# Kernel optimization log

Hardware: AMD Instinct MI355X
Metric: run time of the kernel (lower is better)

## Reference

```python
import jax, jax.numpy as jnp
import numpy as np
import math

H = 1024      # hidden_size
NH = 32       # nhead
DH = H // NH  # head dim (== NH by construction, required for broadcasting)
SF = 0.2      # scaling_factor
B, S = 1, 48  # batch, seq_len (Sq == Sk required)


def setup_inputs() -> dict:
    key = jax.random.key(0)
    ks = jax.random.split(key, 9)
    sd = 1.0 / math.sqrt(H)
    return {
        "q": jax.random.normal(ks[0], (B, S, H), jnp.float32),
        "k": jax.random.normal(ks[1], (B, S, H), jnp.float32),
        "v": jax.random.normal(ks[2], (B, S, H), jnp.float32),
        "Wq": jax.random.normal(ks[3], (H, H), jnp.float32) * sd,
        "bq": jax.random.normal(ks[4], (H,), jnp.float32) * sd,
        "Wk": jax.random.normal(ks[5], (H, H), jnp.float32) * sd,
        "bk": jax.random.normal(ks[6], (H,), jnp.float32) * sd,
        "Wv": jax.random.normal(ks[7], (H, H), jnp.float32) * sd,
        "bv": jax.random.normal(ks[8], (H,), jnp.float32) * sd,
        "dropout_p": 0,
    }


def reference(q, k, v, Wq, bq, Wk, bk, Wv, bv, dropout_p):
    inv_sqrt_h = 1.0 / math.sqrt(H)
    qp = q @ Wq.T + bq  # [B,S,H]
    kp = k @ Wk.T + bk
    vp = v @ Wv.T + bv

    def heads(x):
        # view(-1, S, NH, DH).transpose(0,1) -> [S, B, NH, DH]
        return jnp.swapaxes(x.reshape(-1, x.shape[1], NH, DH), 0, 1)

    qh = heads(qp) * inv_sqrt_h          # [S,B,NH,DH]
    kh = heads(kp)
    vh = heads(vp)

    _sq = jnp.sum(qh * qh, axis=-1)      # [S,B,NH]
    # k^T @ q over the head axis: [S,B,DH,NH] @ [S,B,NH,DH] -> [S,B,DH,DH]
    _sk = jnp.matmul(jnp.swapaxes(kh, -1, -2), qh) * inv_sqrt_h

    # broadcast: [S,B,NH,1] + [S,B,DH,DH,1] + |[S,B,DH,DH]-[S,B,NH,1]|*SF
    # with B=1, DH==NH -> _s: [S,S,NH,NH,NH]
    _s = (_sq[..., None] + _sk[..., None]
          + jnp.abs(jnp.swapaxes(_sk, -1, -2) - _sq[..., None]) * SF)
    attn = jax.nn.softmax(_s, axis=-1)   # [S,S,NH,NH,NH]
    # dropout_p == 0 -> identity (matches `if dropout_p > 0` in torch source)

    out = jnp.matmul(attn, vh)           # batch-broadcast matmul -> [S,S,NH,NH,NH]
    out = jnp.swapaxes(out, 0, 1)
    return out.reshape(out.shape[1], -1)  # [S, S*NH^3]
```

## Files before the change

kernel.cpp:

```cpp
#include <hip/hip_runtime.h>

constexpr int kH  = 1024;
constexpr int kS  = 48;
constexpr int kNH = 32;
constexpr int kDH = 32;
constexpr float kSF = 0.2f;
constexpr int kRepsPerRow = kS * kNH;
constexpr int kRowF4      = kRepsPerRow * 256;

typedef float f32x4 __attribute__((ext_vector_type(4)));

__device__ __forceinline__ float4 ld4(const float* p) {
    return *reinterpret_cast<const float4*>(p);
}
__device__ __forceinline__ float dot4(float4 a, float4 b) {
    return a.x * b.x + a.y * b.y + a.z * b.z + a.w * b.w;
}

__global__ __launch_bounds__(256) void proj_kernel(
    const float* __restrict__ q, const float* __restrict__ k, const float* __restrict__ v,
    const float* __restrict__ Wq, const float* __restrict__ bq,
    const float* __restrict__ Wk, const float* __restrict__ bk,
    const float* __restrict__ Wv, const float* __restrict__ bv,
    float* __restrict__ ws)
{
    const int wid  = blockIdx.x * 4 + (threadIdx.x >> 6);
    const int lane = threadIdx.x & 63;
    const int g = wid >> 10;
    const int o = wid & 1023;

    const float *X, *W, *Bv;
    if (g == 0)      { X = q; W = Wq; Bv = bq; }
    else if (g == 1) { X = k; W = Wk; Bv = bk; }
    else             { X = v; W = Wv; Bv = bv; }
    float* OUT = ws + g * (kS * kH);

    const float* wr = W + o * kH + lane * 4;
    const float4 w0 = ld4(wr);
    const float4 w1 = ld4(wr + 256);
    const float4 w2 = ld4(wr + 512);
    const float4 w3 = ld4(wr + 768);

    float acc[kS];
#pragma unroll
    for (int s = 0; s < kS; ++s) {
        const float* xr = X + s * kH + lane * 4;
        float4 x0 = ld4(xr);
        float4 x1 = ld4(xr + 256);
        float4 x2 = ld4(xr + 512);
        float4 x3 = ld4(xr + 768);
        acc[s] = dot4(x0, w0) + dot4(x1, w1) + dot4(x2, w2) + dot4(x3, w3);
    }
#pragma unroll
    for (int s = 0; s < kS; ++s) {
        float a = acc[s];
        a += __shfl_xor(a, 1);
        a += __shfl_xor(a, 2);
        a += __shfl_xor(a, 4);
        a += __shfl_xor(a, 8);
        a += __shfl_xor(a, 16);
        a += __shfl_xor(a, 32);
        acc[s] = a;
    }
    if (lane == 0) {
        const float bo = Bv[o];
#pragma unroll
        for (int s = 0; s < kS; ++s) OUT[s * kH + o] = acc[s] + bo;
    }
}

__global__ __launch_bounds__(256) void attn_kernel(
    const float* __restrict__ ws, float* __restrict__ O)
{
    const int s = blockIdx.x;
    const int t = threadIdx.x;

    __shared__ float qrow[kH];
    __shared__ float krow[kH];
    __shared__ float vrow[kH];
    __shared__ float sq[kNH];
    __shared__ float sk[kDH][kDH];
    __shared__ float pT[kNH][kNH];

    const float* qp = ws;
    const float* kp = ws + kS * kH;
    const float* vp = ws + 2 * kS * kH;

    reinterpret_cast<float4*>(qrow)[t] = ld4(qp + s * kH + t * 4);
    reinterpret_cast<float4*>(krow)[t] = ld4(kp + s * kH + t * 4);
    reinterpret_cast<float4*>(vrow)[t] = ld4(vp + s * kH + t * 4);
    __syncthreads();

    if (t < kNH) {
        float a = 0.f;
#pragma unroll
        for (int d = 0; d < kDH; ++d) {
            float x = qrow[t * kDH + d];
            a += x * x;
        }
        sq[t] = a * (1.0f / 1024.0f);
    }
    {
        const int d = t >> 3;
        const int eq = t & 7;
        float4 a = {0.f, 0.f, 0.f, 0.f};
#pragma unroll
        for (int n = 0; n < kNH; ++n) {
            const float kv = krow[n * kDH + d];
            const float4 qv = reinterpret_cast<const float4*>(qrow)[n * 8 + eq];
            a.x += kv * qv.x; a.y += kv * qv.y; a.z += kv * qv.z; a.w += kv * qv.w;
        }
        const float sc = 1.0f / 1024.0f;
        a.x *= sc; a.y *= sc; a.z *= sc; a.w *= sc;
        *reinterpret_cast<float4*>(&sk[d][eq * 4]) = a;
    }
    __syncthreads();

    {
        const int b = t >> 3;
        const int c0 = (t & 7) * 4;
        const float s0 = sq[b];
        float v0 = kSF * fabsf(sk[c0 + 0][b] - s0);
        float v1 = kSF * fabsf(sk[c0 + 1][b] - s0);
        float v2 = kSF * fabsf(sk[c0 + 2][b] - s0);
        float v3 = kSF * fabsf(sk[c0 + 3][b] - s0);
        float m = fmaxf(fmaxf(v0, v1), fmaxf(v2, v3));
        m = fmaxf(m, __shfl_xor(m, 1));
        m = fmaxf(m, __shfl_xor(m, 2));
        m = fmaxf(m, __shfl_xor(m, 4));
        float e0 = __expf(v0 - m);
        float e1 = __expf(v1 - m);
        float e2 = __expf(v2 - m);
        float e3 = __expf(v3 - m);
        float sum = e0 + e1 + e2 + e3;
        sum += __shfl_xor(sum, 1);
        sum += __shfl_xor(sum, 2);
        sum += __shfl_xor(sum, 4);
        const float inv = 1.0f / sum;
        pT[c0 + 0][b] = e0 * inv;
        pT[c0 + 1][b] = e1 * inv;
        pT[c0 + 2][b] = e2 * inv;
        pT[c0 + 3][b] = e3 * inv;
    }
    __syncthreads();

    {
        const int b = t >> 3;
        const int dq = t & 7;
        float4 acc = {0.f, 0.f, 0.f, 0.f};
#pragma unroll
        for (int c = 0; c < kNH; ++c) {
            const float pv = pT[c][b];
            const float4 vv = reinterpret_cast<const float4*>(vrow)[c * 8 + dq];
            acc.x += pv * vv.x; acc.y += pv * vv.y; acc.z += pv * vv.z; acc.w += pv * vv.w;
        }
        reinterpret_cast<float4*>(O + s * kH + b * kDH)[dq] = acc;
    }
}

__global__ __launch_bounds__(256) void bcast_kernel(
    const float* __restrict__ O, float* __restrict__ out)
{
    const int x  = blockIdx.x / 96;
    const int rb = blockIdx.x % 96;
    const int t  = threadIdx.x;

    const f32x4 v = *reinterpret_cast<const f32x4*>(O + x * kH + t * 4);
    f32x4* dst = reinterpret_cast<f32x4*>(out)
               + (size_t)x * kRowF4 + (size_t)rb * (16 * 256) + t;
#pragma unroll
    for (int i = 0; i < 16; ++i) {
        __builtin_nontemporal_store(v, dst + i * 256);
    }
}

extern "C" void kernel_launch(void* const* d_in, const int* in_sizes, int n_in,
                              void* d_out, int out_size, void* d_ws, size_t ws_size,
                              hipStream_t stream)
{
    (void)in_sizes; (void)n_in; (void)out_size; (void)ws_size;
    const float* q  = (const float*)d_in[0];
    const float* k  = (const float*)d_in[1];
    const float* v  = (const float*)d_in[2];
    const float* Wq = (const float*)d_in[3];
    const float* bq = (const float*)d_in[4];
    const float* Wk = (const float*)d_in[5];
    const float* bk = (const float*)d_in[6];
    const float* Wv = (const float*)d_in[7];
    const float* bv = (const float*)d_in[8];

    float* ws  = (float*)d_ws;
    float* O   = ws + 3 * kS * kH;
    float* out = (float*)d_out;

    proj_kernel<<<768, 256, 0, stream>>>(q, k, v, Wq, bq, Wk, bk, Wv, bv, ws);
    attn_kernel<<<kS, 256, 0, stream>>>(ws, O);
    bcast_kernel<<<kS * 96, 256, 0, stream>>>(O, out);
}
```

Baseline: 89.69 us.

## Fuse attention into broadcast kernel and tile projection X through shared memory

The projection kernel now stages 128-column tiles of X in shared memory and assigns 32 lanes per output row, so each block computes 8 outputs while reusing the staged X. The attention kernel is merged with the broadcast writer: each of 48*32 blocks recomputes the per-row attention and then writes 48 replicated rows. This removes one launch and the intermediate O buffer. The cost is recomputing attention 32 times per row, and the output stores become ordinary stores instead of nontemporal ones.

```diff
diff --git a/kernel.cpp b/kernel.cpp
--- a/kernel.cpp
+++ b/kernel.cpp
@@ -8,8 +8,6 @@
 constexpr int kRepsPerRow = kS * kNH;
 constexpr int kRowF4      = kRepsPerRow * 256;
 
-typedef float f32x4 __attribute__((ext_vector_type(4)));
-
 __device__ __forceinline__ float4 ld4(const float* p) {
     return *reinterpret_cast<const float4*>(p);
 }
@@ -24,10 +22,12 @@
     const float* __restrict__ Wv, const float* __restrict__ bv,
     float* __restrict__ ws)
 {
-    const int wid  = blockIdx.x * 4 + (threadIdx.x >> 6);
-    const int lane = threadIdx.x & 63;
-    const int g = wid >> 10;
-    const int o = wid & 1023;
+    const int bid = blockIdx.x;
+    const int t = threadIdx.x;
+    const int g = bid >> 7;
+    const int otile = bid & 127;
+    const int o = otile * 8 + (t >> 5);
+    const int kg = t & 31;
 
     const float *X, *W, *Bv;
     if (g == 0)      { X = q; W = Wq; Bv = bq; }
@@ -35,22 +35,31 @@
     else             { X = v; W = Wv; Bv = bv; }
     float* OUT = ws + g * (kS * kH);
 
-    const float* wr = W + o * kH + lane * 4;
-    const float4 w0 = ld4(wr);
-    const float4 w1 = ld4(wr + 256);
-    const float4 w2 = ld4(wr + 512);
-    const float4 w3 = ld4(wr + 768);
+    __shared__ float Xs[kS][128];
 
     float acc[kS];
 #pragma unroll
-    for (int s = 0; s < kS; ++s) {
-        const float* xr = X + s * kH + lane * 4;
-        float4 x0 = ld4(xr);
-        float4 x1 = ld4(xr + 256);
-        float4 x2 = ld4(xr + 512);
-        float4 x3 = ld4(xr + 768);
-        acc[s] = dot4(x0, w0) + dot4(x1, w1) + dot4(x2, w2) + dot4(x3, w3);
-    }
+    for (int s = 0; s < kS; ++s) acc[s] = 0.f;
+
+    for (int kt = 0; kt < 8; ++kt) {
+#pragma unroll
+        for (int r = 0; r < 6; ++r) {
+            const int fi = r * 256 + t;
+            const int s  = fi >> 5;
+            const int c  = fi & 31;
+            reinterpret_cast<float4*>(&Xs[s][0])[c] = ld4(X + s * kH + kt * 128 + c * 4);
+        }
+        __syncthreads();
+
+        const float4 wv = ld4(W + o * kH + kt * 128 + kg * 4);
+#pragma unroll
+        for (int s = 0; s < kS; ++s) {
+            const float4 xv = reinterpret_cast<const float4*>(&Xs[s][0])[kg];
+            acc[s] += dot4(xv, wv);
+        }
+        __syncthreads();
+    }
+
 #pragma unroll
     for (int s = 0; s < kS; ++s) {
         float a = acc[s];
@@ -59,21 +68,21 @@
         a += __shfl_xor(a, 4);
         a += __shfl_xor(a, 8);
         a += __shfl_xor(a, 16);
-        a += __shfl_xor(a, 32);
         acc[s] = a;
     }
-    if (lane == 0) {
+    if (kg == 0) {
         const float bo = Bv[o];
 #pragma unroll
         for (int s = 0; s < kS; ++s) OUT[s * kH + o] = acc[s] + bo;
     }
 }
 
-__global__ __launch_bounds__(256) void attn_kernel(
-    const float* __restrict__ ws, float* __restrict__ O)
+__global__ __launch_bounds__(256) void fused_kernel(
+    const float* __restrict__ ws, float* __restrict__ out)
 {
-    const int s = blockIdx.x;
-    const int t = threadIdx.x;
+    const int x  = blockIdx.x >> 5;
+    const int rb = blockIdx.x & 31;
+    const int t  = threadIdx.x;
 
     __shared__ float qrow[kH];
     __shared__ float krow[kH];
@@ -81,22 +90,23 @@
     __shared__ float sq[kNH];
     __shared__ float sk[kDH][kDH];
     __shared__ float pT[kNH][kNH];
+    __shared__ float Osh[kH];
 
     const float* qp = ws;
     const float* kp = ws + kS * kH;
     const float* vp = ws + 2 * kS * kH;
 
-    reinterpret_cast<float4*>(qrow)[t] = ld4(qp + s * kH + t * 4);
-    reinterpret_cast<float4*>(krow)[t] = ld4(kp + s * kH + t * 4);
-    reinterpret_cast<float4*>(vrow)[t] = ld4(vp + s * kH + t * 4);
+    reinterpret_cast<float4*>(qrow)[t] = ld4(qp + x * kH + t * 4);
+    reinterpret_cast<float4*>(krow)[t] = ld4(kp + x * kH + t * 4);
+    reinterpret_cast<float4*>(vrow)[t] = ld4(vp + x * kH + t * 4);
     __syncthreads();
 
     if (t < kNH) {
         float a = 0.f;
 #pragma unroll
         for (int d = 0; d < kDH; ++d) {
-            float x = qrow[t * kDH + d];
-            a += x * x;
+            float xq = qrow[t * kDH + d];
+            a += xq * xq;
         }
         sq[t] = a * (1.0f / 1024.0f);
     }
@@ -154,23 +164,18 @@
             const float4 vv = reinterpret_cast<const float4*>(vrow)[c * 8 + dq];
             acc.x += pv * vv.x; acc.y += pv * vv.y; acc.z += pv * vv.z; acc.w += pv * vv.w;
         }
-        reinterpret_cast<float4*>(O + s * kH + b * kDH)[dq] = acc;
-    }
-}
-
-__global__ __launch_bounds__(256) void bcast_kernel(
-    const float* __restrict__ O, float* __restrict__ out)
-{
-    const int x  = blockIdx.x / 96;
-    const int rb = blockIdx.x % 96;
-    const int t  = threadIdx.x;
-
-    const f32x4 v = *reinterpret_cast<const f32x4*>(O + x * kH + t * 4);
-    f32x4* dst = reinterpret_cast<f32x4*>(out)
-               + (size_t)x * kRowF4 + (size_t)rb * (16 * 256) + t;
-#pragma unroll
-    for (int i = 0; i < 16; ++i) {
-        __builtin_nontemporal_store(v, dst + i * 256);
+        reinterpret_cast<float4*>(Osh + b * kDH)[dq] = acc;
+    }
+    __syncthreads();
+
+    {
+        const float4 v = reinterpret_cast<const float4*>(Osh)[t];
+        float4* dst = reinterpret_cast<float4*>(out)
+                    + (size_t)x * kRowF4 + (size_t)rb * (48 * 256) + t;
+#pragma unroll
+        for (int i = 0; i < 48; ++i) {
+            dst[i * 256] = v;
+        }
     }
 }
 
@@ -190,10 +195,8 @@
     const float* bv = (const float*)d_in[8];
 
     float* ws  = (float*)d_ws;
-    float* O   = ws + 3 * kS * kH;
     float* out = (float*)d_out;
 
-    proj_kernel<<<768, 256, 0, stream>>>(q, k, v, Wq, bq, Wk, bk, Wv, bv, ws);
-    attn_kernel<<<kS, 256, 0, stream>>>(ws, O);
-    bcast_kernel<<<kS * 96, 256, 0, stream>>>(O, out);
-}
+    proj_kernel<<<384, 256, 0, stream>>>(q, k, v, Wq, bq, Wk, bk, Wv, bv, ws);
+    fused_kernel<<<kS * 32, 256, 0, stream>>>(ws, out);
+}
```

Result: slower. 92.12 us (+2.7%).

## Register-tile projection over outputs and rows, coarsen broadcast with regular stores

Applied to the files above, without the earlier changes.

The projection kernel now gives each wave a 4-output by 12-row tile instead of one output across all 48 rows. Each loaded X vector is reused against four weight rows, which cuts redundant X reads, and the bias add and store are done as float4. The broadcast kernel writes 48 copies per block instead of 16, using a third as many blocks, and switches from nontemporal stores to ordinary stores. The dominant output write of roughly 300MB may behave differently in cache without the nontemporal hint.

```diff
diff --git a/kernel.cpp b/kernel.cpp
--- a/kernel.cpp
+++ b/kernel.cpp
@@ -8,10 +8,11 @@
 constexpr int kRepsPerRow = kS * kNH;
 constexpr int kRowF4      = kRepsPerRow * 256;
 
-typedef float f32x4 __attribute__((ext_vector_type(4)));
-
 __device__ __forceinline__ float4 ld4(const float* p) {
     return *reinterpret_cast<const float4*>(p);
+}
+__device__ __forceinline__ void st4(float* p, float4 v) {
+    *reinterpret_cast<float4*>(p) = v;
 }
 __device__ __forceinline__ float dot4(float4 a, float4 b) {
     return a.x * b.x + a.y * b.y + a.z * b.z + a.w * b.w;
@@ -24,10 +25,14 @@
     const float* __restrict__ Wv, const float* __restrict__ bv,
     float* __restrict__ ws)
 {
-    const int wid  = blockIdx.x * 4 + (threadIdx.x >> 6);
+    const int w    = blockIdx.x * 4 + (threadIdx.x >> 6);
     const int lane = threadIdx.x & 63;
-    const int g = wid >> 10;
-    const int o = wid & 1023;
+    const int g    = w >> 10;
+    const int r    = w & 1023;
+    const int sq   = r >> 8;
+    const int oq   = r & 255;
+    const int s0   = sq * 12;
+    const int o0   = oq * 4;
 
     const float *X, *W, *Bv;
     if (g == 0)      { X = q; W = Wq; Bv = bq; }
@@ -35,37 +40,54 @@
     else             { X = v; W = Wv; Bv = bv; }
     float* OUT = ws + g * (kS * kH);
 
-    const float* wr = W + o * kH + lane * 4;
-    const float4 w0 = ld4(wr);
-    const float4 w1 = ld4(wr + 256);
-    const float4 w2 = ld4(wr + 512);
-    const float4 w3 = ld4(wr + 768);
-
-    float acc[kS];
-#pragma unroll
-    for (int s = 0; s < kS; ++s) {
-        const float* xr = X + s * kH + lane * 4;
-        float4 x0 = ld4(xr);
-        float4 x1 = ld4(xr + 256);
-        float4 x2 = ld4(xr + 512);
-        float4 x3 = ld4(xr + 768);
-        acc[s] = dot4(x0, w0) + dot4(x1, w1) + dot4(x2, w2) + dot4(x3, w3);
-    }
-#pragma unroll
-    for (int s = 0; s < kS; ++s) {
-        float a = acc[s];
-        a += __shfl_xor(a, 1);
-        a += __shfl_xor(a, 2);
-        a += __shfl_xor(a, 4);
-        a += __shfl_xor(a, 8);
-        a += __shfl_xor(a, 16);
-        a += __shfl_xor(a, 32);
-        acc[s] = a;
-    }
+    float acc[4][12];
+#pragma unroll
+    for (int j = 0; j < 4; ++j)
+#pragma unroll
+        for (int s = 0; s < 12; ++s) acc[j][s] = 0.f;
+
+#pragma unroll
+    for (int p = 0; p < 4; ++p) {
+        const int k0 = p * 256 + lane * 4;
+        const float4 w0 = ld4(W + (o0 + 0) * kH + k0);
+        const float4 w1 = ld4(W + (o0 + 1) * kH + k0);
+        const float4 w2 = ld4(W + (o0 + 2) * kH + k0);
+        const float4 w3 = ld4(W + (o0 + 3) * kH + k0);
+#pragma unroll
+        for (int s = 0; s < 12; ++s) {
+            const float4 xv = ld4(X + (s0 + s) * kH + k0);
+            acc[0][s] += dot4(xv, w0);
+            acc[1][s] += dot4(xv, w1);
+            acc[2][s] += dot4(xv, w2);
+            acc[3][s] += dot4(xv, w3);
+        }
+    }
+
+#pragma unroll
+    for (int j = 0; j < 4; ++j)
+#pragma unroll
+        for (int s = 0; s < 12; ++s) {
+            float a = acc[j][s];
+            a += __shfl_xor(a, 1);
+            a += __shfl_xor(a, 2);
+            a += __shfl_xor(a, 4);
+            a += __shfl_xor(a, 8);
+            a += __shfl_xor(a, 16);
+            a += __shfl_xor(a, 32);
+            acc[j][s] = a;
+        }
+
     if (lane == 0) {
-        const float bo = Bv[o];
-#pragma unroll
-        for (int s = 0; s < kS; ++s) OUT[s * kH + o] = acc[s] + bo;
+        const float4 bb = ld4(Bv + o0);
+#pragma unroll
+        for (int s = 0; s < 12; ++s) {
+            float4 o4;
+            o4.x = acc[0][s] + bb.x;
+            o4.y = acc[1][s] + bb.y;
+            o4.z = acc[2][s] + bb.z;
+            o4.w = acc[3][s] + bb.w;
+            st4(OUT + (s0 + s) * kH + o0, o4);
+        }
     }
 }
 
@@ -161,16 +183,16 @@
 __global__ __launch_bounds__(256) void bcast_kernel(
     const float* __restrict__ O, float* __restrict__ out)
 {
-    const int x  = blockIdx.x / 96;
-    const int rb = blockIdx.x % 96;
+    const int x  = blockIdx.x >> 5;
+    const int rb = blockIdx.x & 31;
     const int t  = threadIdx.x;
 
-    const f32x4 v = *reinterpret_cast<const f32x4*>(O + x * kH + t * 4);
-    f32x4* dst = reinterpret_cast<f32x4*>(out)
-               + (size_t)x * kRowF4 + (size_t)rb * (16 * 256) + t;
-#pragma unroll
-    for (int i = 0; i < 16; ++i) {
-        __builtin_nontemporal_store(v, dst + i * 256);
+    const float4 v = ld4(O + x * kH + t * 4);
+    float4* dst = reinterpret_cast<float4*>(out)
+                + (size_t)x * kRowF4 + (size_t)rb * (48 * 256) + t;
+#pragma unroll
+    for (int i = 0; i < 48; ++i) {
+        dst[i * 256] = v;
     }
 }
 
@@ -195,5 +217,5 @@
 
     proj_kernel<<<768, 256, 0, stream>>>(q, k, v, Wq, bq, Wk, bk, Wv, bv, ws);
     attn_kernel<<<kS, 256, 0, stream>>>(ws, O);
-    bcast_kernel<<<kS * 96, 256, 0, stream>>>(O, out);
-}
+    bcast_kernel<<<kS * 32, 256, 0, stream>>>(O, out);
+}
```

Result: slower. 100.8 us (+12.4%).
